# Kernel tuning notes

Hardware: AMD Instinct MI355X
Metric: run time of the kernel (lower is better)

Reference implementation:

```python
import jax, jax.numpy as jnp
import numpy as np

NEG_SLOPE = 0.2  # LeakyReLU slope from the torch module


def setup_inputs() -> dict:
    key = jax.random.key(0)
    k1, k2, k3 = jax.random.split(key, 3)
    B, N, IN = 32, 512, 256
    H, D = 8, 32  # out_dim=256, concat=True -> head_dim = 256 // 8
    x = jax.random.normal(k1, (B, N, IN), dtype=jnp.float32)
    # nn.Linear(in_dim, H*D, bias=False).weight has shape (H*D, in_dim)
    W = jax.random.normal(k2, (H * D, IN), dtype=jnp.float32) * (1.0 / np.sqrt(IN))
    # xavier_uniform on (1, H, 2D)
    limit = float(np.sqrt(6.0 / (H + 2 * D)))
    attn = jax.random.uniform(k3, (1, H, 2 * D), dtype=jnp.float32, minval=-limit, maxval=limit)
    return {"x": x, "W": W, "attn": attn}


def reference(x, W, attn):
    # x: (B, N, IN); W: (H*D, IN); attn: (1, H, 2D)
    B, N, _ = x.shape
    H = attn.shape[1]
    D = attn.shape[2] // 2
    Wx = (x @ W.T).reshape(B, N, H, D)  # (B, N, H, D)
    # Additive attention decomposes: e[b,i,j,h] = leaky(s_src[b,i,h] + s_tgt[b,j,h]).
    # (src = Wx broadcast over j, tgt = Wx broadcast over i; cat*attn sums split in two.)
    a_src = attn[0, :, :D]  # (H, D)
    a_tgt = attn[0, :, D:]  # (H, D)
    s_src = jnp.einsum('bnhd,hd->bnh', Wx, a_src)
    s_tgt = jnp.einsum('bnhd,hd->bnh', Wx, a_tgt)
    e = jax.nn.leaky_relu(s_src[:, :, None, :] + s_tgt[:, None, :, :], NEG_SLOPE)  # (B,N,N,H)
    a = jax.nn.softmax(e, axis=2)  # softmax over source nodes j
    # dropout p=0 (eval mode) -> identity
    out = jnp.einsum('bijh,bjhd->bihd', a, Wx)  # (B, N, H, D)
    out = out.reshape(B, N, H * D)  # concat=True
    return jax.nn.elu(out)
```

## Files before the change

kernel.cpp:

```cpp
#include <hip/hip_runtime.h>
#include <math.h>

#define NEG_SLOPE 0.2f
#define LOG2E 1.44269504088896f

#if __has_builtin(__builtin_amdgcn_exp2f)
#define EXP2F __builtin_amdgcn_exp2f
#else
#define EXP2F exp2f
#endif

typedef _Float16 f16x8 __attribute__((ext_vector_type(8)));
typedef float f32x4 __attribute__((ext_vector_type(4)));

union PK8 { uint4 u4; _Float16 h[8]; };
union PK1 { unsigned short u; _Float16 h; };

#define XN_CHUNKS (32 * 512 * 256 / 8)
#define WN_CHUNKS (256 * 256 / 8)

__global__ __launch_bounds__(256) void cvt_f16(const float* __restrict__ x,
                                               const float* __restrict__ W,
                                               unsigned short* __restrict__ xf,
                                               unsigned short* __restrict__ wf) {
    int idx = blockIdx.x * 256 + threadIdx.x;
    const float* src;
    unsigned short* dst;
    if (idx < XN_CHUNKS) {
        src = x + (size_t)idx * 8;
        dst = xf + (size_t)idx * 8;
    } else {
        int j = idx - XN_CHUNKS;
        if (j >= WN_CHUNKS) return;
        src = W + (size_t)j * 8;
        dst = wf + (size_t)j * 8;
    }
    float4 v0 = *(const float4*)(src);
    float4 v1 = *(const float4*)(src + 4);
    PK8 p;
    p.h[0] = (_Float16)v0.x; p.h[1] = (_Float16)v0.y;
    p.h[2] = (_Float16)v0.z; p.h[3] = (_Float16)v0.w;
    p.h[4] = (_Float16)v1.x; p.h[5] = (_Float16)v1.y;
    p.h[6] = (_Float16)v1.z; p.h[7] = (_Float16)v1.w;
    *(uint4*)dst = p.u4;
}

__global__ __launch_bounds__(256) void gemm_wxt(const unsigned short* __restrict__ xf,
                                                const unsigned short* __restrict__ wf,
                                                unsigned short* __restrict__ wxtg) {
    __shared__ __align__(16) unsigned short xs[64 * 64];
    __shared__ __align__(16) unsigned short pool[128 * 64];
    unsigned short* ws = pool;
    unsigned short* tb = pool;

    const int tid = threadIdx.x;
    const int bid = blockIdx.x;
    const int m0 = (bid >> 1) * 64;
    const int n0 = (bid & 1) * 128;
    const int w = tid >> 6, l = tid & 63;
    const int q = l >> 4, ln = l & 15;
    const int iw = (w & 1) * 32, nw = (w >> 1) * 64;

    f32x4 acc[2][4];
    #pragma unroll
    for (int g = 0; g < 2; ++g)
        #pragma unroll
        for (int t = 0; t < 4; ++t) acc[g][t] = (f32x4){0.f, 0.f, 0.f, 0.f};

    for (int kc = 0; kc < 256; kc += 64) {
        __syncthreads();
        #pragma unroll
        for (int p = 0; p < 2; ++p) {
            int idx = p * 256 + tid;
            int row = idx >> 3, c = idx & 7;
            uint4 v = *(const uint4*)(xf + (size_t)(m0 + row) * 256 + kc + c * 8);
            *(uint4*)((char*)xs + ((row * 128 + c * 16) ^ ((row & 7) << 4))) = v;
        }
        #pragma unroll
        for (int p = 0; p < 4; ++p) {
            int idx = p * 256 + tid;
            int n = idx >> 3, c = idx & 7;
            uint4 v = *(const uint4*)(wf + (size_t)(n0 + n) * 256 + kc + c * 8);
            *(uint4*)((char*)ws + ((n * 128 + c * 16) ^ ((n & 7) << 4))) = v;
        }
        __syncthreads();

        #pragma unroll
        for (int ks = 0; ks < 2; ++ks) {
            const int kb = ks * 64 + q * 16;
            f16x8 af[2];
            #pragma unroll
            for (int g = 0; g < 2; ++g) {
                int row = iw + g * 16 + ln;
                uint4 raw = *(const uint4*)((const char*)xs +
                            ((row * 128 + kb) ^ ((row & 7) << 4)));
                PK8 pk; pk.u4 = raw;
                af[g] = *(f16x8*)&pk;
            }
            #pragma unroll
            for (int t = 0; t < 4; ++t) {
                int n = nw + t * 16 + ln;
                uint4 raw = *(const uint4*)((const char*)ws +
                            ((n * 128 + kb) ^ ((n & 7) << 4)));
                PK8 pk; pk.u4 = raw;
                f16x8 bf = *(f16x8*)&pk;
                acc[0][t] = __builtin_amdgcn_mfma_f32_16x16x32_f16(af[0], bf, acc[0][t], 0, 0, 0);
                acc[1][t] = __builtin_amdgcn_mfma_f32_16x16x32_f16(af[1], bf, acc[1][t], 0, 0, 0);
            }
        }
    }

    __syncthreads();
    #pragma unroll
    for (int g = 0; g < 2; ++g)
        #pragma unroll
        for (int t = 0; t < 4; ++t)
            #pragma unroll
            for (int r = 0; r < 4; ++r) {
                int n  = nw + t * 16 + ln;
                int jl = iw + g * 16 + q * 4 + r;
                PK1 hv; hv.h = (_Float16)acc[g][t][r];
                *(unsigned short*)((char*)tb + ((n * 128 + jl * 2) ^ ((n & 7) << 4))) = hv.u;
            }
    __syncthreads();
    {
        const int b = m0 >> 9, j0 = m0 & 511;
        #pragma unroll
        for (int p = 0; p < 4; ++p) {
            int idx = p * 256 + tid;
            int n = idx >> 3, c = idx & 7;
            uint4 v = *(const uint4*)((const char*)tb + ((n * 128 + c * 16) ^ ((n & 7) << 4)));
            int nn = n0 + n;
            *(uint4*)(wxtg + ((size_t)(b * 256 + nn) * 512 + j0 + c * 8)) = v;
        }
    }
}

__global__ __launch_bounds__(512, 4) void gat_attn(const unsigned short* __restrict__ wxtg,
                                                   const float* __restrict__ attn,
                                                   float* __restrict__ out) {
    __shared__ __align__(16) unsigned short wxt[32 * 512];
    __shared__ float stf[512];
    __shared__ float ssrc[512];
    __shared__ float red_s[8];

    const int bid = blockIdx.x;
    const int bh = bid & 255, half = bid >> 8;
    const int b = bh >> 3, h = bh & 7;
    const int tid = threadIdx.x;
    const int w = tid >> 6, l = tid & 63;
    const int q = l >> 4, ln = l & 15;

    {
        const unsigned short* src = wxtg + (size_t)bh * 32 * 512;
        const int d = tid >> 4, cs = tid & 15;
        #pragma unroll
        for (int p = 0; p < 4; ++p) {
            int c = p * 16 + cs;
            uint4 v = *(const uint4*)(src + d * 512 + c * 8);
            *(uint4*)((char*)wxt + ((d * 1024 + c * 16) ^ ((d & 7) << 4))) = v;
        }
    }
    __syncthreads();

    {
        const int j = tid;
        float ss = 0.f, st = 0.f;
        #pragma unroll
        for (int d = 0; d < 32; ++d) {
            PK1 hv;
            hv.u = *(const unsigned short*)((const char*)wxt +
                    ((d * 1024 + j * 2) ^ ((d & 7) << 4)));
            float v = (float)hv.h;
            ss += v * attn[h * 64 + d];
            st += v * attn[h * 64 + 32 + d];
        }
        ssrc[j] = ss * LOG2E;
        float stv = st * LOG2E;
        stf[j] = stv;
        float m = stv;
        #pragma unroll
        for (int off = 32; off > 0; off >>= 1)
            m = fmaxf(m, __shfl_xor(m, off));
        if (l == 0) red_s[w] = m;
    }
    __syncthreads();
    float maxtK = red_s[0];
    #pragma unroll
    for (int ww = 1; ww < 8; ++ww) maxtK = fmaxf(maxtK, red_s[ww]);

    const int ibase = half * 256 + w * 32;
    float ciK[2], miK[2];
    #pragma unroll
    for (int g = 0; g < 2; ++g) {
        float cc = ssrc[ibase + g * 16 + ln];
        float cm = cc + maxtK;
        miK[g] = fmaxf(cm, NEG_SLOPE * cm);
        ciK[g] = cc;
    }

    f32x4 acc[2][2];
    #pragma unroll
    for (int g = 0; g < 2; ++g) {
        acc[g][0] = (f32x4){0.f, 0.f, 0.f, 0.f};
        acc[g][1] = (f32x4){0.f, 0.f, 0.f, 0.f};
    }
    float pd[2] = {0.f, 0.f};

    for (int kk = 0; kk < 16; ++kk) {
        const int j0 = kk * 32 + q * 8;
        float4 s0 = *(const float4*)(stf + j0);
        float4 s1 = *(const float4*)(stf + j0 + 4);
        float st[8] = {s0.x, s0.y, s0.z, s0.w, s1.x, s1.y, s1.z, s1.w};

        f16x8 bf[2];
        #pragma unroll
        for (int dt = 0; dt < 2; ++dt) {
            int d = dt * 16 + ln;
            int bb = d * 1024 + kk * 64 + q * 16;
            uint4 raw = *(const uint4*)((const char*)wxt + (bb ^ ((d & 7) << 4)));
            PK8 pk; pk.u4 = raw;
            bf[dt] = *(f16x8*)&pk;
        }

        #pragma unroll
        for (int g = 0; g < 2; ++g) {
            f16x8 pa;
            float s = 0.f;
            #pragma unroll
            for (int e = 0; e < 8; ++e) {
                float eK = ciK[g] + st[e];
                float lr = fmaxf(eK, NEG_SLOPE * eK);
                float p = EXP2F(lr - miK[g]);
                s += p;
                pa[e] = (_Float16)p;
            }
            pd[g] += s;
            acc[g][0] = __builtin_amdgcn_mfma_f32_16x16x32_f16(pa, bf[0], acc[g][0], 0, 0, 0);
            acc[g][1] = __builtin_amdgcn_mfma_f32_16x16x32_f16(pa, bf[1], acc[g][1], 0, 0, 0);
        }
    }

    float inv[2];
    #pragma unroll
    for (int g = 0; g < 2; ++g) {
        float s = pd[g];
        s += __shfl_xor(s, 16);
        s += __shfl_xor(s, 32);
        inv[g] = 1.f / s;
    }
    #pragma unroll
    for (int g = 0; g < 2; ++g)
        #pragma unroll
        for (int dt = 0; dt < 2; ++dt)
            #pragma unroll
            for (int r = 0; r < 4; ++r) {
                int row = q * 4 + r;
                float dn = __shfl(inv[g], row);
                float o = acc[g][dt][r] * dn;
                o = o > 0.f ? o : (__expf(o) - 1.f);
                size_t i = (size_t)(b * 512 + ibase + g * 16 + row);
                out[i * 256 + h * 32 + dt * 16 + ln] = o;
            }
}

extern "C" void kernel_launch(void* const* d_in, const int* in_sizes, int n_in,
                              void* d_out, int out_size, void* d_ws, size_t ws_size,
                              hipStream_t stream) {
    const float* x    = (const float*)d_in[0];
    const float* W    = (const float*)d_in[1];
    const float* attn = (const float*)d_in[2];
    float* out = (float*)d_out;

    unsigned short* xf   = (unsigned short*)d_ws;
    unsigned short* wf   = xf + (size_t)32 * 512 * 256;
    unsigned short* wxtg = wf + 256 * 256;

    cvt_f16<<<(XN_CHUNKS + WN_CHUNKS + 255) / 256, 256, 0, stream>>>(x, W, xf, wf);
    gemm_wxt<<<512, 256, 0, stream>>>(xf, wf, wxtg);
    gat_attn<<<512, 512, 0, stream>>>(wxtg, attn, out);
}
```

Baseline: 39.24 us.

## Fuse x fp16 conversion into GEMM loads and pack softmax math into vector pairs

Result: slower. 41.89 us (+6.8%).

```diff
diff --git a/kernel.cpp b/kernel.cpp
--- a/kernel.cpp
+++ b/kernel.cpp
@@ -11,41 +11,32 @@
 #endif
 
 typedef _Float16 f16x8 __attribute__((ext_vector_type(8)));
+typedef __fp16 h16x2 __attribute__((ext_vector_type(2)));
 typedef float f32x4 __attribute__((ext_vector_type(4)));
-
-union PK8 { uint4 u4; _Float16 h[8]; };
+typedef float f32x2 __attribute__((ext_vector_type(2)));
+
+union PK8 { uint4 u4; _Float16 h[8]; f16x8 v; h16x2 p[4]; };
+union PKH { h16x2 v; unsigned int u; unsigned short s[2]; };
 union PK1 { unsigned short u; _Float16 h; };
 
-#define XN_CHUNKS (32 * 512 * 256 / 8)
 #define WN_CHUNKS (256 * 256 / 8)
 
-__global__ __launch_bounds__(256) void cvt_f16(const float* __restrict__ x,
-                                               const float* __restrict__ W,
-                                               unsigned short* __restrict__ xf,
-                                               unsigned short* __restrict__ wf) {
+__global__ __launch_bounds__(256) void cvt_w(const float* __restrict__ W,
+                                             unsigned short* __restrict__ wf) {
     int idx = blockIdx.x * 256 + threadIdx.x;
-    const float* src;
-    unsigned short* dst;
-    if (idx < XN_CHUNKS) {
-        src = x + (size_t)idx * 8;
-        dst = xf + (size_t)idx * 8;
-    } else {
-        int j = idx - XN_CHUNKS;
-        if (j >= WN_CHUNKS) return;
-        src = W + (size_t)j * 8;
-        dst = wf + (size_t)j * 8;
-    }
+    if (idx >= WN_CHUNKS) return;
+    const float* src = W + (size_t)idx * 8;
     float4 v0 = *(const float4*)(src);
     float4 v1 = *(const float4*)(src + 4);
     PK8 p;
-    p.h[0] = (_Float16)v0.x; p.h[1] = (_Float16)v0.y;
-    p.h[2] = (_Float16)v0.z; p.h[3] = (_Float16)v0.w;
-    p.h[4] = (_Float16)v1.x; p.h[5] = (_Float16)v1.y;
-    p.h[6] = (_Float16)v1.z; p.h[7] = (_Float16)v1.w;
-    *(uint4*)dst = p.u4;
-}
-
-__global__ __launch_bounds__(256) void gemm_wxt(const unsigned short* __restrict__ xf,
+    p.p[0] = __builtin_amdgcn_cvt_pkrtz(v0.x, v0.y);
+    p.p[1] = __builtin_amdgcn_cvt_pkrtz(v0.z, v0.w);
+    p.p[2] = __builtin_amdgcn_cvt_pkrtz(v1.x, v1.y);
+    p.p[3] = __builtin_amdgcn_cvt_pkrtz(v1.z, v1.w);
+    *(uint4*)(wf + (size_t)idx * 8) = p.u4;
+}
+
+__global__ __launch_bounds__(256) void gemm_wxt(const float* __restrict__ x,
                                                 const unsigned short* __restrict__ wf,
                                                 unsigned short* __restrict__ wxtg) {
     __shared__ __align__(16) unsigned short xs[64 * 64];
@@ -55,8 +46,8 @@
 
     const int tid = threadIdx.x;
     const int bid = blockIdx.x;
-    const int m0 = (bid >> 1) * 64;
-    const int n0 = (bid & 1) * 128;
+    const int m0 = (bid & 255) * 64;
+    const int n0 = (bid >> 8) * 128;
     const int w = tid >> 6, l = tid & 63;
     const int q = l >> 4, ln = l & 15;
     const int iw = (w & 1) * 32, nw = (w >> 1) * 64;
@@ -69,12 +60,25 @@
 
     for (int kc = 0; kc < 256; kc += 64) {
         __syncthreads();
-        #pragma unroll
-        for (int p = 0; p < 2; ++p) {
-            int idx = p * 256 + tid;
-            int row = idx >> 3, c = idx & 7;
-            uint4 v = *(const uint4*)(xf + (size_t)(m0 + row) * 256 + kc + c * 8);
-            *(uint4*)((char*)xs + ((row * 128 + c * 16) ^ ((row & 7) << 4))) = v;
+        {
+            const int i = tid >> 2, kq = tid & 3;
+            const float* src = x + (size_t)(m0 + i) * 256 + kc + kq * 16;
+            float4 v0 = *(const float4*)(src + 0);
+            float4 v1 = *(const float4*)(src + 4);
+            float4 v2 = *(const float4*)(src + 8);
+            float4 v3 = *(const float4*)(src + 12);
+            PK8 p0, p1;
+            p0.p[0] = __builtin_amdgcn_cvt_pkrtz(v0.x, v0.y);
+            p0.p[1] = __builtin_amdgcn_cvt_pkrtz(v0.z, v0.w);
+            p0.p[2] = __builtin_amdgcn_cvt_pkrtz(v1.x, v1.y);
+            p0.p[3] = __builtin_amdgcn_cvt_pkrtz(v1.z, v1.w);
+            p1.p[0] = __builtin_amdgcn_cvt_pkrtz(v2.x, v2.y);
+            p1.p[1] = __builtin_amdgcn_cvt_pkrtz(v2.z, v2.w);
+            p1.p[2] = __builtin_amdgcn_cvt_pkrtz(v3.x, v3.y);
+            p1.p[3] = __builtin_amdgcn_cvt_pkrtz(v3.z, v3.w);
+            int b0 = i * 128 + kq * 32;
+            *(uint4*)((char*)xs + (b0 ^ ((i & 7) << 4))) = p0.u4;
+            *(uint4*)((char*)xs + ((b0 + 16) ^ ((i & 7) << 4))) = p1.u4;
         }
         #pragma unroll
         for (int p = 0; p < 4; ++p) {
@@ -95,7 +99,7 @@
                 uint4 raw = *(const uint4*)((const char*)xs +
                             ((row * 128 + kb) ^ ((row & 7) << 4)));
                 PK8 pk; pk.u4 = raw;
-                af[g] = *(f16x8*)&pk;
+                af[g] = pk.v;
             }
             #pragma unroll
             for (int t = 0; t < 4; ++t) {
@@ -103,7 +107,7 @@
                 uint4 raw = *(const uint4*)((const char*)ws +
                             ((n * 128 + kb) ^ ((n & 7) << 4)));
                 PK8 pk; pk.u4 = raw;
-                f16x8 bf = *(f16x8*)&pk;
+                f16x8 bf = pk.v;
                 acc[0][t] = __builtin_amdgcn_mfma_f32_16x16x32_f16(af[0], bf, acc[0][t], 0, 0, 0);
                 acc[1][t] = __builtin_amdgcn_mfma_f32_16x16x32_f16(af[1], bf, acc[1][t], 0, 0, 0);
             }
@@ -205,13 +209,20 @@
         acc[g][0] = (f32x4){0.f, 0.f, 0.f, 0.f};
         acc[g][1] = (f32x4){0.f, 0.f, 0.f, 0.f};
     }
-    float pd[2] = {0.f, 0.f};
-
+    f32x2 pdv[2] = {(f32x2){0.f, 0.f}, (f32x2){0.f, 0.f}};
+
+    #pragma unroll 2
     for (int kk = 0; kk < 16; ++kk) {
         const int j0 = kk * 32 + q * 8;
-        float4 s0 = *(const float4*)(stf + j0);
-        float4 s1 = *(const float4*)(stf + j0 + 4);
-        float st[8] = {s0.x, s0.y, s0.z, s0.w, s1.x, s1.y, s1.z, s1.w};
+        f32x2 stp[4];
+        {
+            float4 s0 = *(const float4*)(stf + j0);
+            float4 s1 = *(const float4*)(stf + j0 + 4);
+            stp[0] = (f32x2){s0.x, s0.y};
+            stp[1] = (f32x2){s0.z, s0.w};
+            stp[2] = (f32x2){s1.x, s1.y};
+            stp[3] = (f32x2){s1.z, s1.w};
+        }
 
         f16x8 bf[2];
         #pragma unroll
@@ -220,31 +231,35 @@
             int bb = d * 1024 + kk * 64 + q * 16;
             uint4 raw = *(const uint4*)((const char*)wxt + (bb ^ ((d & 7) << 4)));
             PK8 pk; pk.u4 = raw;
-            bf[dt] = *(f16x8*)&pk;
+            bf[dt] = pk.v;
         }
 
         #pragma unroll
         for (int g = 0; g < 2; ++g) {
-            f16x8 pa;
-            float s = 0.f;
-            #pragma unroll
-            for (int e = 0; e < 8; ++e) {
-                float eK = ciK[g] + st[e];
-                float lr = fmaxf(eK, NEG_SLOPE * eK);
-                float p = EXP2F(lr - miK[g]);
-                s += p;
-                pa[e] = (_Float16)p;
-            }
-            pd[g] += s;
-            acc[g][0] = __builtin_amdgcn_mfma_f32_16x16x32_f16(pa, bf[0], acc[g][0], 0, 0, 0);
-            acc[g][1] = __builtin_amdgcn_mfma_f32_16x16x32_f16(pa, bf[1], acc[g][1], 0, 0, 0);
+            const f32x2 ci2 = (f32x2){ciK[g], ciK[g]};
+            const f32x2 mi2 = (f32x2){miK[g], miK[g]};
+            PK8 pa;
+            #pragma unroll
+            for (int pr = 0; pr < 4; ++pr) {
+                f32x2 e  = ci2 + stp[pr];
+                f32x2 a1 = e - mi2;
+                f32x2 a2 = (f32x2){NEG_SLOPE, NEG_SLOPE} * e - mi2;
+                float m0 = fmaxf(a1.x, a2.x);
+                float m1 = fmaxf(a1.y, a2.y);
+                float p0 = EXP2F(m0);
+                float p1 = EXP2F(m1);
+                pdv[g] += (f32x2){p0, p1};
+                pa.p[pr] = __builtin_amdgcn_cvt_pkrtz(p0, p1);
+            }
+            acc[g][0] = __builtin_amdgcn_mfma_f32_16x16x32_f16(pa.v, bf[0], acc[g][0], 0, 0, 0);
+            acc[g][1] = __builtin_amdgcn_mfma_f32_16x16x32_f16(pa.v, bf[1], acc[g][1], 0, 0, 0);
         }
     }
 
     float inv[2];
     #pragma unroll
     for (int g = 0; g < 2; ++g) {
-        float s = pd[g];
+        float s = pdv[g].x + pdv[g].y;
         s += __shfl_xor(s, 16);
         s += __shfl_xor(s, 32);
         inv[g] = 1.f / s;
@@ -272,11 +287,10 @@
     const float* attn = (const float*)d_in[2];
     float* out = (float*)d_out;
 
-    unsigned short* xf   = (unsigned short*)d_ws;
-    unsigned short* wf   = xf + (size_t)32 * 512 * 256;
+    unsigned short* wf   = (unsigned short*)d_ws;
     unsigned short* wxtg = wf + 256 * 256;
 
-    cvt_f16<<<(XN_CHUNKS + WN_CHUNKS + 255) / 256, 256, 0, stream>>>(x, W, xf, wf);
-    gemm_wxt<<<512, 256, 0, stream>>>(xf, wf, wxtg);
+    cvt_w<<<WN_CHUNKS / 256, 256, 0, stream>>>(W, wf);
+    gemm_wxt<<<512, 256, 0, stream>>>(x, wf, wxtg);
     gat_attn<<<512, 512, 0, stream>>>(wxtg, attn, out);
 }
```

## Compute attention scores in GEMM epilogue and use packed f16 conversion

Applied to the files above, without the earlier changes.

New measurement: 41.90 us. 1.07x slower.

```diff
diff --git a/kernel.cpp b/kernel.cpp
--- a/kernel.cpp
+++ b/kernel.cpp
@@ -11,9 +11,10 @@
 #endif
 
 typedef _Float16 f16x8 __attribute__((ext_vector_type(8)));
+typedef __fp16 h16x2 __attribute__((ext_vector_type(2)));
 typedef float f32x4 __attribute__((ext_vector_type(4)));
 
-union PK8 { uint4 u4; _Float16 h[8]; };
+union PK8 { uint4 u4; _Float16 h[8]; f16x8 v; h16x2 p[4]; };
 union PK1 { unsigned short u; _Float16 h; };
 
 #define XN_CHUNKS (32 * 512 * 256 / 8)
@@ -38,16 +39,19 @@
     float4 v0 = *(const float4*)(src);
     float4 v1 = *(const float4*)(src + 4);
     PK8 p;
-    p.h[0] = (_Float16)v0.x; p.h[1] = (_Float16)v0.y;
-    p.h[2] = (_Float16)v0.z; p.h[3] = (_Float16)v0.w;
-    p.h[4] = (_Float16)v1.x; p.h[5] = (_Float16)v1.y;
-    p.h[6] = (_Float16)v1.z; p.h[7] = (_Float16)v1.w;
+    p.p[0] = __builtin_amdgcn_cvt_pkrtz(v0.x, v0.y);
+    p.p[1] = __builtin_amdgcn_cvt_pkrtz(v0.z, v0.w);
+    p.p[2] = __builtin_amdgcn_cvt_pkrtz(v1.x, v1.y);
+    p.p[3] = __builtin_amdgcn_cvt_pkrtz(v1.z, v1.w);
     *(uint4*)dst = p.u4;
 }
 
 __global__ __launch_bounds__(256) void gemm_wxt(const unsigned short* __restrict__ xf,
                                                 const unsigned short* __restrict__ wf,
-                                                unsigned short* __restrict__ wxtg) {
+                                                const float* __restrict__ attn,
+                                                unsigned short* __restrict__ wxtg,
+                                                float* __restrict__ s_src,
+                                                float* __restrict__ s_tgt) {
     __shared__ __align__(16) unsigned short xs[64 * 64];
     __shared__ __align__(16) unsigned short pool[128 * 64];
     unsigned short* ws = pool;
@@ -95,7 +99,7 @@
                 uint4 raw = *(const uint4*)((const char*)xs +
                             ((row * 128 + kb) ^ ((row & 7) << 4)));
                 PK8 pk; pk.u4 = raw;
-                af[g] = *(f16x8*)&pk;
+                af[g] = pk.v;
             }
             #pragma unroll
             for (int t = 0; t < 4; ++t) {
@@ -103,11 +107,48 @@
                 uint4 raw = *(const uint4*)((const char*)ws +
                             ((n * 128 + kb) ^ ((n & 7) << 4)));
                 PK8 pk; pk.u4 = raw;
-                f16x8 bf = *(f16x8*)&pk;
+                f16x8 bf = pk.v;
                 acc[0][t] = __builtin_amdgcn_mfma_f32_16x16x32_f16(af[0], bf, acc[0][t], 0, 0, 0);
                 acc[1][t] = __builtin_amdgcn_mfma_f32_16x16x32_f16(af[1], bf, acc[1][t], 0, 0, 0);
             }
         }
+    }
+
+    {
+        const int h0 = (n0 + nw) >> 5;
+        float avs[2][2], avt[2][2];
+        #pragma unroll
+        for (int hh = 0; hh < 2; ++hh)
+            #pragma unroll
+            for (int t = 0; t < 2; ++t) {
+                avs[hh][t] = attn[(h0 + hh) * 64 + t * 16 + ln];
+                avt[hh][t] = attn[(h0 + hh) * 64 + 32 + t * 16 + ln];
+            }
+        const int bb8 = (m0 >> 9) * 8;
+        const int jbase = (m0 & 511) + iw;
+        #pragma unroll
+        for (int g = 0; g < 2; ++g)
+            #pragma unroll
+            for (int r = 0; r < 4; ++r) {
+                float ps0 = acc[g][0][r] * avs[0][0] + acc[g][1][r] * avs[0][1];
+                float pt0 = acc[g][0][r] * avt[0][0] + acc[g][1][r] * avt[0][1];
+                float ps1 = acc[g][2][r] * avs[1][0] + acc[g][3][r] * avs[1][1];
+                float pt1 = acc[g][2][r] * avt[1][0] + acc[g][3][r] * avt[1][1];
+                #pragma unroll
+                for (int off = 1; off < 16; off <<= 1) {
+                    ps0 += __shfl_xor(ps0, off);
+                    pt0 += __shfl_xor(pt0, off);
+                    ps1 += __shfl_xor(ps1, off);
+                    pt1 += __shfl_xor(pt1, off);
+                }
+                if (ln == 0) {
+                    int j = jbase + g * 16 + q * 4 + r;
+                    s_src[(bb8 + h0) * 512 + j] = ps0;
+                    s_tgt[(bb8 + h0) * 512 + j] = pt0;
+                    s_src[(bb8 + h0 + 1) * 512 + j] = ps1;
+                    s_tgt[(bb8 + h0 + 1) * 512 + j] = pt1;
+                }
+            }
     }
 
     __syncthreads();
@@ -137,11 +178,11 @@
 }
 
 __global__ __launch_bounds__(512, 4) void gat_attn(const unsigned short* __restrict__ wxtg,
-                                                   const float* __restrict__ attn,
+                                                   const float* __restrict__ s_src,
+                                                   const float* __restrict__ s_tgt,
                                                    float* __restrict__ out) {
     __shared__ __align__(16) unsigned short wxt[32 * 512];
     __shared__ float stf[512];
-    __shared__ float ssrc[512];
     __shared__ float red_s[8];
 
     const int bid = blockIdx.x;
@@ -161,23 +202,9 @@
             *(uint4*)((char*)wxt + ((d * 1024 + c * 16) ^ ((d & 7) << 4))) = v;
         }
     }
-    __syncthreads();
-
     {
-        const int j = tid;
-        float ss = 0.f, st = 0.f;
-        #pragma unroll
-        for (int d = 0; d < 32; ++d) {
-            PK1 hv;
-            hv.u = *(const unsigned short*)((const char*)wxt +
-                    ((d * 1024 + j * 2) ^ ((d & 7) << 4)));
-            float v = (float)hv.h;
-            ss += v * attn[h * 64 + d];
-            st += v * attn[h * 64 + 32 + d];
-        }
-        ssrc[j] = ss * LOG2E;
-        float stv = st * LOG2E;
-        stf[j] = stv;
+        float stv = s_tgt[bh * 512 + tid] * LOG2E;
+        stf[tid] = stv;
         float m = stv;
         #pragma unroll
         for (int off = 32; off > 0; off >>= 1)
@@ -193,7 +220,7 @@
     float ciK[2], miK[2];
     #pragma unroll
     for (int g = 0; g < 2; ++g) {
-        float cc = ssrc[ibase + g * 16 + ln];
+        float cc = s_src[bh * 512 + ibase + g * 16 + ln] * LOG2E;
         float cm = cc + maxtK;
         miK[g] = fmaxf(cm, NEG_SLOPE * cm);
         ciK[g] = cc;
@@ -220,7 +247,7 @@
             int bb = d * 1024 + kk * 64 + q * 16;
             uint4 raw = *(const uint4*)((const char*)wxt + (bb ^ ((d & 7) << 4)));
             PK8 pk; pk.u4 = raw;
-            bf[dt] = *(f16x8*)&pk;
+            bf[dt] = pk.v;
         }
 
         #pragma unroll
@@ -259,7 +286,7 @@
                 float dn = __shfl(inv[g], row);
                 float o = acc[g][dt][r] * dn;
                 o = o > 0.f ? o : (__expf(o) - 1.f);
-                size_t i = (size_t)(b * 512 + ibase + g * 16 + row);
+                size_t i = (size_t)(b * 512 + half * 256 + w * 32 + g * 16 + row);
                 out[i * 256 + h * 32 + dt * 16 + ln] = o;
             }
 }
@@ -275,8 +302,10 @@
     unsigned short* xf   = (unsigned short*)d_ws;
     unsigned short* wf   = xf + (size_t)32 * 512 * 256;
     unsigned short* wxtg = wf + 256 * 256;
+    float* s_src = (float*)(wxtg + (size_t)256 * 32 * 512);
+    float* s_tgt = s_src + 256 * 512;
 
     cvt_f16<<<(XN_CHUNKS + WN_CHUNKS + 255) / 256, 256, 0, stream>>>(x, W, xf, wf);
-    gemm_wxt<<<512, 256, 0, stream>>>(xf, wf, wxtg);
-    gat_attn<<<512, 512, 0, stream>>>(wxtg, attn, out);
+    gemm_wxt<<<512, 256, 0, stream>>>(xf, wf, attn, wxtg, s_src, s_tgt);
+    gat_attn<<<512, 512, 0, stream>>>(wxtg, s_src, s_tgt, out);
 }
```
